# Kernel tuning notes

Measured on AMD Instinct MI355X. Metric: run time of the kernel, lower is better.

The kernel has to match this reference:

```python
import jax, jax.numpy as jnp
import numpy as np

N, E, D, IN_DIM, NUM_CLASSES, G, L = 50000, 800000, 128, 128, 10, 64, 3
BN_EPS = 1e-5


def _bn(h, gamma, beta, mean, var):
    # inference-mode batchnorm with running stats
    return (h - mean) * jax.lax.rsqrt(var + BN_EPS) * gamma + beta


def setup_inputs() -> dict:
    key = jax.random.key(0)
    ks = jax.random.split(key, 24)
    s = 0.02
    x = jax.random.normal(ks[0], (N, IN_DIM), dtype=jnp.float32)
    c_2 = jax.random.randint(ks[1], (E,), 0, N)
    u_2 = jax.random.randint(ks[2], (E,), 0, N)
    batch = jnp.sort(jax.random.randint(ks[3], (N,), 0, G))
    inp = {
        "x": x, "c_2": c_2, "u_2": u_2, "batch": batch,
        "We": jax.random.normal(ks[4], (IN_DIM, D)) * s,
        "be": jnp.zeros((D,), jnp.float32),
        # per-layer GIN MLP: Linear(d,2d) -> BN(2d) -> ReLU -> Linear(2d,d)
        "W1": jax.random.normal(ks[5], (L, D, 2 * D)) * s,
        "b1": jnp.zeros((L, 2 * D), jnp.float32),
        "g1": jnp.ones((L, 2 * D), jnp.float32),
        "bt1": jnp.zeros((L, 2 * D), jnp.float32),
        "m1": jax.random.normal(ks[6], (L, 2 * D)) * 0.1,
        "v1": jax.random.uniform(ks[7], (L, 2 * D), minval=0.5, maxval=1.5),
        "W2": jax.random.normal(ks[8], (L, 2 * D, D)) * s,
        "b2": jnp.zeros((L, D), jnp.float32),
        # post-conv BatchNorm(d)
        "g2": jnp.ones((L, D), jnp.float32),
        "bt2": jnp.zeros((L, D), jnp.float32),
        "m2": jax.random.normal(ks[9], (L, D)) * 0.1,
        "v2": jax.random.uniform(ks[10], (L, D), minval=0.5, maxval=1.5),
        # readout: Linear(d,d) -> ReLU -> (dropout off) -> Linear(d,num_classes)
        "Wr1": jax.random.normal(ks[11], (D, D)) * s,
        "br1": jnp.zeros((D,), jnp.float32),
        "Wr2": jax.random.normal(ks[12], (D, NUM_CLASSES)) * s,
        "br2": jnp.zeros((NUM_CLASSES,), jnp.float32),
    }
    return inp


def reference(x, c_2, u_2, batch, We, be, W1, b1, g1, bt1, m1, v1,
              W2, b2, g2, bt2, m2, v2, Wr1, br1, Wr2, br2):
    h = x @ We + be  # [N, D]
    for l in range(L):
        # GINConv (eps=0): h_i <- MLP(h_i + sum_{j->i} h_j)
        agg = jax.ops.segment_sum(h[c_2], u_2, num_segments=N)  # [N, D]
        z = h + agg
        z = jax.nn.relu(_bn(z @ W1[l] + b1[l], g1[l], bt1[l], m1[l], v1[l]))
        z = z @ W2[l] + b2[l]
        h = jax.nn.relu(_bn(z, g2[l], bt2[l], m2[l], v2[l]))
        # dropout: identity in eval mode
    pooled = jax.ops.segment_sum(h, batch, num_segments=G)  # [G, D]
    out = jax.nn.relu(pooled @ Wr1 + br1) @ Wr2 + br2  # [G, num_classes]
    return out
```

## Files before the change

kernel.cpp:

```cpp
#include <hip/hip_runtime.h>

#define BN_EPS 1e-5f

typedef __attribute__((ext_vector_type(8))) short bf16x8;
typedef __attribute__((ext_vector_type(4))) float f32x4;
typedef unsigned int uint32;

__device__ __forceinline__ unsigned short f2bf(float f) {
    unsigned u = __float_as_uint(f);
    u += 0x7FFFu + ((u >> 16) & 1u);
    return (unsigned short)(u >> 16);
}
__device__ __forceinline__ float bf2f(unsigned short u) {
    return __uint_as_float((unsigned)u << 16);
}
__device__ __forceinline__ float lo_bf(uint32 u) { return __uint_as_float(u << 16); }
__device__ __forceinline__ float hi_bf(uint32 u) { return __uint_as_float(u & 0xFFFF0000u); }
__device__ __forceinline__ uint32 pack_bf(float a0, float a1) {
    return ((uint32)f2bf(a1) << 16) | (uint32)f2bf(a0);
}

__global__ __launch_bounds__(256) void count_coarse_kernel(const int* __restrict__ u2,
                                                           int* __restrict__ coarse_cnt, int E) {
    __shared__ int lcnt[256];
    const int tid = threadIdx.x;
    lcnt[tid] = 0;
    __syncthreads();
    const int e0 = blockIdx.x * 4096;
#pragma unroll
    for (int k = 0; k < 16; ++k) {
        int e = e0 + k * 256 + tid;
        if (e < E) atomicAdd(&lcnt[u2[e] >> 8], 1);
    }
    __syncthreads();
    int c = lcnt[tid];
    if (c) atomicAdd(&coarse_cnt[tid], c);
}

__global__ __launch_bounds__(256) void scan_coarse_kernel(const int* __restrict__ coarse_cnt,
                                                          int* __restrict__ coarse_start,
                                                          int* __restrict__ coarse_cursor,
                                                          int nc, int total) {
    __shared__ int buf[256];
    const int t = threadIdx.x;
    int v = (t < nc) ? coarse_cnt[t] : 0;
    buf[t] = v;
    __syncthreads();
    for (int off = 1; off < 256; off <<= 1) {
        int x = (t >= off) ? buf[t - off] : 0;
        __syncthreads();
        buf[t] += x;
        __syncthreads();
    }
    int excl = buf[t] - v;
    if (t <= nc) coarse_start[t] = (t < nc) ? excl : total;
    if (t < nc) coarse_cursor[t] = excl;
}

__global__ __launch_bounds__(256) void bin_coarse_kernel(const int* __restrict__ u2,
                                                         const int* __restrict__ c2,
                                                         int* __restrict__ coarse_cursor,
                                                         int* __restrict__ buck, int E) {
    __shared__ int lcnt[256];
    __shared__ int lbase[256];
    const int tid = threadIdx.x;
    lcnt[tid] = 0;
    __syncthreads();
    const int e0 = blockIdx.x * 4096;
    int ue[16];
#pragma unroll
    for (int k = 0; k < 16; ++k) {
        int e = e0 + k * 256 + tid;
        int u = (e < E) ? u2[e] : -1;
        ue[k] = u;
        if (u >= 0) atomicAdd(&lcnt[u >> 8], 1);
    }
    __syncthreads();
    int c0 = lcnt[tid];
    lbase[tid] = c0 ? atomicAdd(&coarse_cursor[tid], c0) : 0;
    lcnt[tid] = 0;
    __syncthreads();
#pragma unroll
    for (int k = 0; k < 16; ++k) {
        int e = e0 + k * 256 + tid;
        if (e < E) {
            int u = ue[k];
            int cb = u >> 8;
            int pos = lbase[cb] + atomicAdd(&lcnt[cb], 1);
            buck[pos] = ((u & 255) << 16) | c2[e];
        }
    }
}

__global__ __launch_bounds__(256) void bin_node_kernel(const int* __restrict__ coarse_start,
                                                       const int* __restrict__ buck,
                                                       int* __restrict__ node_start,
                                                       int* __restrict__ csr_src, int N) {
    __shared__ int lcnt[256];
    __shared__ int lcur[256];
    const int cb = blockIdx.x;
    const int tid = threadIdx.x;
    const int s = coarse_start[cb];
    const int t_end = coarse_start[cb + 1];
    lcnt[tid] = 0;
    __syncthreads();
    for (int e = s + tid; e < t_end; e += 256)
        atomicAdd(&lcnt[buck[e] >> 16], 1);
    __syncthreads();
    int v = lcnt[tid];
    lcur[tid] = v;
    __syncthreads();
    for (int off = 1; off < 256; off <<= 1) {
        int x = (tid >= off) ? lcur[tid - off] : 0;
        __syncthreads();
        lcur[tid] += x;
        __syncthreads();
    }
    int excl = lcur[tid] - v;
    int gstart = s + excl;
    int idx = cb * 256 + tid;
    if (idx <= N) node_start[idx] = gstart;
    lcur[tid] = gstart;
    __syncthreads();
    for (int e = s + tid; e < t_end; e += 256) {
        int w = buck[e];
        int pos = atomicAdd(&lcur[w >> 16], 1);
        csr_src[pos] = w & 0xFFFF;
    }
}

__global__ __launch_bounds__(256) void aggregate_kernel(const unsigned short* __restrict__ h,
                                                        const int* __restrict__ row_start,
                                                        const int* __restrict__ csr_src,
                                                        unsigned short* __restrict__ h2, int N) {
    int node = blockIdx.x * 4 + (threadIdx.x >> 6);
    int lane = threadIdx.x & 63;
    if (node >= N) return;
    const int q = lane >> 4, sl = lane & 15;

    float a0 = 0.f, a1 = 0.f, a2 = 0.f, a3 = 0.f, a4 = 0.f, a5 = 0.f, a6 = 0.f, a7 = 0.f;
    if (q == 0) {
        uint4 v = ((const uint4*)(h + (size_t)node * 128))[sl];
        a0 = lo_bf(v.x); a1 = hi_bf(v.x); a2 = lo_bf(v.y); a3 = hi_bf(v.y);
        a4 = lo_bf(v.z); a5 = hi_bf(v.z); a6 = lo_bf(v.w); a7 = hi_bf(v.w);
    }

    const int rs = row_start[node], re = row_start[node + 1];
    int e = rs;
    for (; e + 16 <= re; e += 16) {
        int s0 = csr_src[e + q];
        int s1 = csr_src[e + 4 + q];
        int s2 = csr_src[e + 8 + q];
        int s3 = csr_src[e + 12 + q];
        uint4 v0 = ((const uint4*)(h + (size_t)s0 * 128))[sl];
        uint4 v1 = ((const uint4*)(h + (size_t)s1 * 128))[sl];
        uint4 v2 = ((const uint4*)(h + (size_t)s2 * 128))[sl];
        uint4 v3 = ((const uint4*)(h + (size_t)s3 * 128))[sl];
        a0 += (lo_bf(v0.x) + lo_bf(v1.x)) + (lo_bf(v2.x) + lo_bf(v3.x));
        a1 += (hi_bf(v0.x) + hi_bf(v1.x)) + (hi_bf(v2.x) + hi_bf(v3.x));
        a2 += (lo_bf(v0.y) + lo_bf(v1.y)) + (lo_bf(v2.y) + lo_bf(v3.y));
        a3 += (hi_bf(v0.y) + hi_bf(v1.y)) + (hi_bf(v2.y) + hi_bf(v3.y));
        a4 += (lo_bf(v0.z) + lo_bf(v1.z)) + (lo_bf(v2.z) + lo_bf(v3.z));
        a5 += (hi_bf(v0.z) + hi_bf(v1.z)) + (hi_bf(v2.z) + hi_bf(v3.z));
        a6 += (lo_bf(v0.w) + lo_bf(v1.w)) + (lo_bf(v2.w) + lo_bf(v3.w));
        a7 += (hi_bf(v0.w) + hi_bf(v1.w)) + (hi_bf(v2.w) + hi_bf(v3.w));
    }
    for (; e + 8 <= re; e += 8) {
        int s0 = csr_src[e + q];
        int s1 = csr_src[e + 4 + q];
        uint4 v = ((const uint4*)(h + (size_t)s0 * 128))[sl];
        uint4 w = ((const uint4*)(h + (size_t)s1 * 128))[sl];
        a0 += lo_bf(v.x) + lo_bf(w.x); a1 += hi_bf(v.x) + hi_bf(w.x);
        a2 += lo_bf(v.y) + lo_bf(w.y); a3 += hi_bf(v.y) + hi_bf(w.y);
        a4 += lo_bf(v.z) + lo_bf(w.z); a5 += hi_bf(v.z) + hi_bf(w.z);
        a6 += lo_bf(v.w) + lo_bf(w.w); a7 += hi_bf(v.w) + hi_bf(w.w);
    }
    for (; e + 4 <= re; e += 4) {
        int s0 = csr_src[e + q];
        uint4 v = ((const uint4*)(h + (size_t)s0 * 128))[sl];
        a0 += lo_bf(v.x); a1 += hi_bf(v.x); a2 += lo_bf(v.y); a3 += hi_bf(v.y);
        a4 += lo_bf(v.z); a5 += hi_bf(v.z); a6 += lo_bf(v.w); a7 += hi_bf(v.w);
    }
    if (q < re - e) {
        int s0 = csr_src[e + q];
        uint4 v = ((const uint4*)(h + (size_t)s0 * 128))[sl];
        a0 += lo_bf(v.x); a1 += hi_bf(v.x); a2 += lo_bf(v.y); a3 += hi_bf(v.y);
        a4 += lo_bf(v.z); a5 += hi_bf(v.z); a6 += lo_bf(v.w); a7 += hi_bf(v.w);
    }

    a0 += __shfl_xor(a0, 16, 64); a0 += __shfl_xor(a0, 32, 64);
    a1 += __shfl_xor(a1, 16, 64); a1 += __shfl_xor(a1, 32, 64);
    a2 += __shfl_xor(a2, 16, 64); a2 += __shfl_xor(a2, 32, 64);
    a3 += __shfl_xor(a3, 16, 64); a3 += __shfl_xor(a3, 32, 64);
    a4 += __shfl_xor(a4, 16, 64); a4 += __shfl_xor(a4, 32, 64);
    a5 += __shfl_xor(a5, 16, 64); a5 += __shfl_xor(a5, 32, 64);
    a6 += __shfl_xor(a6, 16, 64); a6 += __shfl_xor(a6, 32, 64);
    a7 += __shfl_xor(a7, 16, 64); a7 += __shfl_xor(a7, 32, 64);

    if (q == 0) {
        uint4 o;
        o.x = pack_bf(a0, a1); o.y = pack_bf(a2, a3);
        o.z = pack_bf(a4, a5); o.w = pack_bf(a6, a7);
        ((uint4*)(h2 + (size_t)node * 128))[sl] = o;
    }
}

__global__ void prep_kernel(const float* __restrict__ We, const float* __restrict__ W1,
                            const float* __restrict__ W2,
                            unsigned short* __restrict__ Wte,
                            unsigned short* __restrict__ Wt1,
                            unsigned short* __restrict__ Wt2,
                            const float* __restrict__ be,
                            const float* __restrict__ b1, const float* __restrict__ g1,
                            const float* __restrict__ bt1, const float* __restrict__ m1,
                            const float* __restrict__ v1,
                            const float* __restrict__ b2, const float* __restrict__ g2,
                            const float* __restrict__ bt2, const float* __restrict__ m2,
                            const float* __restrict__ v2,
                            float* __restrict__ sce, float* __restrict__ she,
                            float* __restrict__ sc1, float* __restrict__ sh1,
                            float* __restrict__ sc2, float* __restrict__ sh2, int L) {
    int y = blockIdx.y;
    int t = threadIdx.x;
    if (blockIdx.x == 0) {
        if (y == 0) {
            if (t < 128) { sce[t] = 1.f; she[t] = be[t]; }
        } else if (y <= L) {
            int o = (y - 1) * 256 + t;
            float s = g1[o] * rsqrtf(v1[o] + BN_EPS);
            sc1[o] = s;
            sh1[o] = (b1[o] - m1[o]) * s + bt1[o];
        } else {
            if (t < 128) {
                int o = (y - L - 1) * 128 + t;
                float s = g2[o] * rsqrtf(v2[o] + BN_EPS);
                sc2[o] = s;
                sh2[o] = (b2[o] - m2[o]) * s + bt2[o];
            }
        }
    }
    const float* src;
    unsigned short* dst;
    int K;
    if (y == 0)      { src = We; dst = Wte; K = 128; }
    else if (y <= L) { int l = y - 1;     src = W1 + (size_t)l * 128 * 256; dst = Wt1 + (size_t)l * 128 * 256; K = 128; }
    else             { int l = y - L - 1; src = W2 + (size_t)l * 256 * 128; dst = Wt2 + (size_t)l * 256 * 128; K = 256; }
    int idx = blockIdx.x * 256 + t;
    int OUT = 32768 / K;
    if (y == 0) { if (idx >= 128 * 128) return; OUT = 128; }
    int c = idx / K, k = idx % K;
    unsigned byte = ((unsigned)(idx * 2)) ^ (((unsigned)c & 7u) << 4);
    *(unsigned short*)((char*)dst + byte) = f2bf(src[(size_t)k * OUT + c]);
}

template <int K, int OUT, bool RELU, bool A_F32>
__global__ __launch_bounds__(256) void mfma_gemm_kernel(
    const void* __restrict__ Ap, const unsigned short* __restrict__ Wt,
    const float* __restrict__ scale, const float* __restrict__ shift,
    unsigned short* __restrict__ Cout, int nrows)
{
    constexpr int NT = OUT / 16;
    constexpr int KS = K / 32;
    constexpr int CH = OUT * K / 8;
    __shared__ unsigned short WtLds[OUT * K];

    const int tid = threadIdx.x;
    const int wv = tid >> 6, lane = tid & 63;
    {
#pragma unroll
        for (int i = 0; i < CH / 256; ++i) {
            unsigned chunk = (unsigned)(i * 256 + wv * 64);
            const char* gsrc = (const char*)Wt + (size_t)(chunk + lane) * 16u;
            char* ldst = (char*)WtLds + (size_t)chunk * 16u;
            __builtin_amdgcn_global_load_lds(
                (const __attribute__((address_space(1))) void*)gsrc,
                (__attribute__((address_space(3))) void*)ldst,
                16, 0, 0);
        }
    }

    const int l15 = lane & 15, lhi = lane >> 4;
    const int rbase = blockIdx.x * 128 + wv * 32;
    const int r0 = rbase + l15;
    const int r1 = rbase + 16 + l15;
    const int rr0 = min(r0, nrows - 1);
    const int rr1 = min(r1, nrows - 1);

    bf16x8 bfrag[2][KS];
    if constexpr (A_F32) {
        const float* a0 = (const float*)Ap + (size_t)rr0 * K + lhi * 8;
        const float* a1 = (const float*)Ap + (size_t)rr1 * K + lhi * 8;
#pragma unroll
        for (int ks = 0; ks < KS; ++ks) {
            float4 u0 = *(const float4*)(a0 + ks * 32);
            float4 u1 = *(const float4*)(a0 + ks * 32 + 4);
            float4 w0 = *(const float4*)(a1 + ks * 32);
            float4 w1 = *(const float4*)(a1 + ks * 32 + 4);
            bf16x8 f, g;
            f[0] = (short)f2bf(u0.x); f[1] = (short)f2bf(u0.y);
            f[2] = (short)f2bf(u0.z); f[3] = (short)f2bf(u0.w);
            f[4] = (short)f2bf(u1.x); f[5] = (short)f2bf(u1.y);
            f[6] = (short)f2bf(u1.z); f[7] = (short)f2bf(u1.w);
            g[0] = (short)f2bf(w0.x); g[1] = (short)f2bf(w0.y);
            g[2] = (short)f2bf(w0.z); g[3] = (short)f2bf(w0.w);
            g[4] = (short)f2bf(w1.x); g[5] = (short)f2bf(w1.y);
            g[6] = (short)f2bf(w1.z); g[7] = (short)f2bf(w1.w);
            bfrag[0][ks] = f;
            bfrag[1][ks] = g;
        }
    } else {
        const unsigned short* a0 = (const unsigned short*)Ap + (size_t)rr0 * K + lhi * 8;
        const unsigned short* a1 = (const unsigned short*)Ap + (size_t)rr1 * K + lhi * 8;
#pragma unroll
        for (int ks = 0; ks < KS; ++ks) {
            bfrag[0][ks] = *(const bf16x8*)(a0 + ks * 32);
            bfrag[1][ks] = *(const bf16x8*)(a1 + ks * 32);
        }
    }

    __syncthreads();

    f32x4 acc[2][NT];
#pragma unroll
    for (int g = 0; g < 2; ++g)
#pragma unroll
        for (int nt = 0; nt < NT; ++nt) acc[g][nt] = (f32x4){0.f, 0.f, 0.f, 0.f};

#pragma unroll
    for (int ks = 0; ks < KS; ++ks) {
#pragma unroll
        for (int nt = 0; nt < NT; ++nt) {
            int row = nt * 16 + l15;
            unsigned off = ((unsigned)((row * K + ks * 32 + lhi * 8) * 2)) ^ (((unsigned)(l15 & 7u)) << 4);
            bf16x8 wfrag = *(const bf16x8*)((const char*)WtLds + off);
            acc[0][nt] = __builtin_amdgcn_mfma_f32_16x16x32_bf16(wfrag, bfrag[0][ks], acc[0][nt], 0, 0, 0);
            acc[1][nt] = __builtin_amdgcn_mfma_f32_16x16x32_bf16(wfrag, bfrag[1][ks], acc[1][nt], 0, 0, 0);
        }
    }

    const float4* sc4 = (const float4*)scale;
    const float4* sh4 = (const float4*)shift;
#pragma unroll
    for (int g = 0; g < 2; ++g) {
        const int r = (g == 0) ? r0 : r1;
        if (r >= nrows) continue;
#pragma unroll
        for (int nt = 0; nt < NT; ++nt) {
            float4 sc = sc4[nt * 4 + lhi];
            float4 sh = sh4[nt * 4 + lhi];
            float y0 = acc[g][nt][0] * sc.x + sh.x;
            float y1 = acc[g][nt][1] * sc.y + sh.y;
            float y2 = acc[g][nt][2] * sc.z + sh.z;
            float y3 = acc[g][nt][3] * sc.w + sh.w;
            if (RELU) {
                y0 = fmaxf(y0, 0.f); y1 = fmaxf(y1, 0.f);
                y2 = fmaxf(y2, 0.f); y3 = fmaxf(y3, 0.f);
            }
            size_t o = (size_t)r * OUT + nt * 16 + lhi * 4;
            ushort4 p = make_ushort4(f2bf(y0), f2bf(y1), f2bf(y2), f2bf(y3));
            *(ushort4*)(Cout + o) = p;
        }
    }
}

__global__ __launch_bounds__(128) void pool_kernel(const unsigned short* __restrict__ h,
                                                   const int* __restrict__ batch,
                                                   float* __restrict__ pooled, int N, int chunk) {
    int d = threadIdx.x;
    int start = blockIdx.x * chunk;
    if (start >= N) return;
    int end = min(start + chunk, N);
    float acc = 0.f;
    int g = batch[start];
    for (int r = start; r < end; ++r) {
        int bg = batch[r];
        if (bg != g) {
            atomicAdd(&pooled[g * 128 + d], acc);
            acc = 0.f;
            g = bg;
        }
        acc += bf2f(h[(size_t)r * 128 + d]);
    }
    atomicAdd(&pooled[g * 128 + d], acc);
}

__global__ __launch_bounds__(128) void readout_kernel(const float* __restrict__ pooled,
                                                      const float* __restrict__ Wr1,
                                                      const float* __restrict__ br1,
                                                      const float* __restrict__ Wr2,
                                                      const float* __restrict__ br2,
                                                      float* __restrict__ out) {
    __shared__ float prow[128];
    __shared__ float t[128];
    int g = blockIdx.x, j = threadIdx.x;
    prow[j] = pooled[g * 128 + j];
    __syncthreads();
    float acc = 0.f;
    for (int k = 0; k < 128; ++k) acc += prow[k] * Wr1[k * 128 + j];
    t[j] = fmaxf(acc + br1[j], 0.f);
    __syncthreads();
    if (j < 10) {
        float a2 = 0.f;
        for (int k = 0; k < 128; ++k) a2 += t[k] * Wr2[k * 10 + j];
        out[g * 10 + j] = a2 + br2[j];
    }
}

extern "C" void kernel_launch(void* const* d_in, const int* in_sizes, int n_in,
                              void* d_out, int out_size, void* d_ws, size_t ws_size,
                              hipStream_t stream) {
    const float* x   = (const float*)d_in[0];
    const int* c2    = (const int*)d_in[1];
    const int* u2    = (const int*)d_in[2];
    const int* batch = (const int*)d_in[3];
    const float* We  = (const float*)d_in[4];
    const float* be  = (const float*)d_in[5];
    const float* W1  = (const float*)d_in[6];
    const float* b1  = (const float*)d_in[7];
    const float* g1  = (const float*)d_in[8];
    const float* bt1 = (const float*)d_in[9];
    const float* m1  = (const float*)d_in[10];
    const float* v1  = (const float*)d_in[11];
    const float* W2  = (const float*)d_in[12];
    const float* b2  = (const float*)d_in[13];
    const float* g2  = (const float*)d_in[14];
    const float* bt2 = (const float*)d_in[15];
    const float* m2  = (const float*)d_in[16];
    const float* v2  = (const float*)d_in[17];
    const float* Wr1 = (const float*)d_in[18];
    const float* br1 = (const float*)d_in[19];
    const float* Wr2 = (const float*)d_in[20];
    const float* br2 = (const float*)d_in[21];

    const int N = in_sizes[3];
    const int E = in_sizes[1];
    const int L = in_sizes[7] / 256;
    const int G = out_size / 10;

    const int NC = (N + 255) / 256;

    char* ws = (char*)d_ws;
    size_t off = 0;
    auto alloc = [&](size_t bytes) { char* p = ws + off; off += (bytes + 255) & ~(size_t)255; return p; };
    unsigned short* hb   = (unsigned short*)alloc((size_t)N * 128 * 2);
    unsigned short* h2b  = (unsigned short*)alloc((size_t)N * 128 * 2);
    unsigned short* zb   = (unsigned short*)alloc((size_t)N * 256 * 2);
    unsigned short* Wte  = (unsigned short*)alloc(128 * 128 * 2);
    unsigned short* Wt1  = (unsigned short*)alloc((size_t)L * 256 * 128 * 2);
    unsigned short* Wt2  = (unsigned short*)alloc((size_t)L * 128 * 256 * 2);
    float* sce = (float*)alloc(128 * 4);
    float* she = (float*)alloc(128 * 4);
    float* sc1 = (float*)alloc((size_t)L * 256 * 4);
    float* sh1 = (float*)alloc((size_t)L * 256 * 4);
    float* sc2 = (float*)alloc((size_t)L * 128 * 4);
    float* sh2 = (float*)alloc((size_t)L * 128 * 4);
    float* pooled = (float*)alloc((size_t)G * 128 * 4);
    int* coarse_cnt    = (int*)alloc(256 * 4);
    int* coarse_start  = (int*)alloc(257 * 4);
    int* coarse_cursor = (int*)alloc(256 * 4);
    int* node_start    = (int*)alloc((size_t)(N + 1) * 4);
    int* buck          = (int*)alloc((size_t)E * 4);
    int* csr_src       = (int*)alloc((size_t)E * 4);

    const int ebins = (E + 4095) / 4096;

    hipMemsetAsync(coarse_cnt, 0, 256 * 4, stream);
    hipMemsetAsync(pooled, 0, (size_t)G * 128 * 4, stream);
    count_coarse_kernel<<<ebins, 256, 0, stream>>>(u2, coarse_cnt, E);
    scan_coarse_kernel<<<1, 256, 0, stream>>>(coarse_cnt, coarse_start, coarse_cursor, NC, E);
    bin_coarse_kernel<<<ebins, 256, 0, stream>>>(u2, c2, coarse_cursor, buck, E);
    bin_node_kernel<<<NC, 256, 0, stream>>>(coarse_start, buck, node_start, csr_src, N);

    prep_kernel<<<dim3((256 * 128 + 255) / 256, 1 + 2 * L), 256, 0, stream>>>(
        We, W1, W2, Wte, Wt1, Wt2,
        be, b1, g1, bt1, m1, v1, b2, g2, bt2, m2, v2,
        sce, she, sc1, sh1, sc2, sh2, L);

    const int gemm_blocks = (N + 127) / 128;

    mfma_gemm_kernel<128, 128, false, true><<<gemm_blocks, 256, 0, stream>>>(
        x, Wte, sce, she, hb, N);

    for (int l = 0; l < L; ++l) {
        aggregate_kernel<<<(N + 3) / 4, 256, 0, stream>>>(hb, node_start, csr_src, h2b, N);
        mfma_gemm_kernel<128, 256, true, false><<<gemm_blocks, 256, 0, stream>>>(
            h2b, Wt1 + (size_t)l * 128 * 256, sc1 + l * 256, sh1 + l * 256, zb, N);
        mfma_gemm_kernel<256, 128, true, false><<<gemm_blocks, 256, 0, stream>>>(
            zb, Wt2 + (size_t)l * 256 * 128, sc2 + l * 128, sh2 + l * 128, hb, N);
    }

    const int pool_blocks = 2048;
    const int chunk = (N + pool_blocks - 1) / pool_blocks;
    pool_kernel<<<pool_blocks, 128, 0, stream>>>(hb, batch, pooled, N, chunk);
    readout_kernel<<<G, 128, 0, stream>>>(pooled, Wr1, br1, Wr2, br2, (float*)d_out);
}
```

Before: 277.6 us.

## Fuse neighbor aggregation into first MLP GEMM and drop the scan kernel

Neighbor aggregation now runs inside the first GEMM kernel. Each lane gathers and sums its row's neighbor features directly into MFMA B-fragments, so the h2b intermediate is no longer written and re-read. The separate coarse-scan kernel is removed, and each binning block redoes the small 256-entry scan itself. The cost is a gather with lower memory parallelism: one lane walks each node's edges serially, with far fewer rows per block than the wave-per-node aggregate. That may hurt latency hiding.

```diff
diff --git a/kernel.cpp b/kernel.cpp
--- a/kernel.cpp
+++ b/kernel.cpp
@@ -18,6 +18,13 @@
 __device__ __forceinline__ float hi_bf(uint32 u) { return __uint_as_float(u & 0xFFFF0000u); }
 __device__ __forceinline__ uint32 pack_bf(float a0, float a1) {
     return ((uint32)f2bf(a1) << 16) | (uint32)f2bf(a0);
+}
+
+__device__ __forceinline__ void acc8(float (&a)[8], uint4 v) {
+    a[0] += lo_bf(v.x); a[1] += hi_bf(v.x);
+    a[2] += lo_bf(v.y); a[3] += hi_bf(v.y);
+    a[4] += lo_bf(v.z); a[5] += hi_bf(v.z);
+    a[6] += lo_bf(v.w); a[7] += hi_bf(v.w);
 }
 
 __global__ __launch_bounds__(256) void count_coarse_kernel(const int* __restrict__ u2,
@@ -37,33 +44,25 @@
     if (c) atomicAdd(&coarse_cnt[tid], c);
 }
 
-__global__ __launch_bounds__(256) void scan_coarse_kernel(const int* __restrict__ coarse_cnt,
-                                                          int* __restrict__ coarse_start,
-                                                          int* __restrict__ coarse_cursor,
-                                                          int nc, int total) {
-    __shared__ int buf[256];
-    const int t = threadIdx.x;
-    int v = (t < nc) ? coarse_cnt[t] : 0;
-    buf[t] = v;
-    __syncthreads();
-    for (int off = 1; off < 256; off <<= 1) {
-        int x = (t >= off) ? buf[t - off] : 0;
-        __syncthreads();
-        buf[t] += x;
-        __syncthreads();
-    }
-    int excl = buf[t] - v;
-    if (t <= nc) coarse_start[t] = (t < nc) ? excl : total;
-    if (t < nc) coarse_cursor[t] = excl;
-}
-
 __global__ __launch_bounds__(256) void bin_coarse_kernel(const int* __restrict__ u2,
                                                          const int* __restrict__ c2,
-                                                         int* __restrict__ coarse_cursor,
-                                                         int* __restrict__ buck, int E) {
+                                                         const int* __restrict__ coarse_cnt,
+                                                         int* __restrict__ coarse_alloc,
+                                                         int* __restrict__ buck, int E, int nc) {
+    __shared__ int sbuf[256];
     __shared__ int lcnt[256];
     __shared__ int lbase[256];
     const int tid = threadIdx.x;
+    int cv = (tid < nc) ? coarse_cnt[tid] : 0;
+    sbuf[tid] = cv;
+    __syncthreads();
+    for (int off = 1; off < 256; off <<= 1) {
+        int x = (tid >= off) ? sbuf[tid - off] : 0;
+        __syncthreads();
+        sbuf[tid] += x;
+        __syncthreads();
+    }
+    const int cstart = sbuf[tid] - cv;
     lcnt[tid] = 0;
     __syncthreads();
     const int e0 = blockIdx.x * 4096;
@@ -77,7 +76,7 @@
     }
     __syncthreads();
     int c0 = lcnt[tid];
-    lbase[tid] = c0 ? atomicAdd(&coarse_cursor[tid], c0) : 0;
+    lbase[tid] = cstart + (c0 ? atomicAdd(&coarse_alloc[tid], c0) : 0);
     lcnt[tid] = 0;
     __syncthreads();
 #pragma unroll
@@ -92,18 +91,28 @@
     }
 }
 
-__global__ __launch_bounds__(256) void bin_node_kernel(const int* __restrict__ coarse_start,
+__global__ __launch_bounds__(256) void bin_node_kernel(const int* __restrict__ coarse_cnt,
                                                        const int* __restrict__ buck,
                                                        int* __restrict__ node_start,
-                                                       int* __restrict__ csr_src, int N) {
+                                                       int* __restrict__ csr_src, int N, int nc) {
+    __shared__ int sbuf[256];
     __shared__ int lcnt[256];
     __shared__ int lcur[256];
     const int cb = blockIdx.x;
     const int tid = threadIdx.x;
-    const int s = coarse_start[cb];
-    const int t_end = coarse_start[cb + 1];
+    int cv = (tid < nc) ? coarse_cnt[tid] : 0;
+    sbuf[tid] = cv;
+    __syncthreads();
+    for (int off = 1; off < 256; off <<= 1) {
+        int x = (tid >= off) ? sbuf[tid - off] : 0;
+        __syncthreads();
+        sbuf[tid] += x;
+        __syncthreads();
+    }
     lcnt[tid] = 0;
     __syncthreads();
+    const int s = (cb == 0) ? 0 : sbuf[cb - 1];
+    const int t_end = sbuf[cb];
     for (int e = s + tid; e < t_end; e += 256)
         atomicAdd(&lcnt[buck[e] >> 16], 1);
     __syncthreads();
@@ -126,82 +135,6 @@
         int w = buck[e];
         int pos = atomicAdd(&lcur[w >> 16], 1);
         csr_src[pos] = w & 0xFFFF;
-    }
-}
-
-__global__ __launch_bounds__(256) void aggregate_kernel(const unsigned short* __restrict__ h,
-                                                        const int* __restrict__ row_start,
-                                                        const int* __restrict__ csr_src,
-                                                        unsigned short* __restrict__ h2, int N) {
-    int node = blockIdx.x * 4 + (threadIdx.x >> 6);
-    int lane = threadIdx.x & 63;
-    if (node >= N) return;
-    const int q = lane >> 4, sl = lane & 15;
-
-    float a0 = 0.f, a1 = 0.f, a2 = 0.f, a3 = 0.f, a4 = 0.f, a5 = 0.f, a6 = 0.f, a7 = 0.f;
-    if (q == 0) {
-        uint4 v = ((const uint4*)(h + (size_t)node * 128))[sl];
-        a0 = lo_bf(v.x); a1 = hi_bf(v.x); a2 = lo_bf(v.y); a3 = hi_bf(v.y);
-        a4 = lo_bf(v.z); a5 = hi_bf(v.z); a6 = lo_bf(v.w); a7 = hi_bf(v.w);
-    }
-
-    const int rs = row_start[node], re = row_start[node + 1];
-    int e = rs;
-    for (; e + 16 <= re; e += 16) {
-        int s0 = csr_src[e + q];
-        int s1 = csr_src[e + 4 + q];
-        int s2 = csr_src[e + 8 + q];
-        int s3 = csr_src[e + 12 + q];
-        uint4 v0 = ((const uint4*)(h + (size_t)s0 * 128))[sl];
-        uint4 v1 = ((const uint4*)(h + (size_t)s1 * 128))[sl];
-        uint4 v2 = ((const uint4*)(h + (size_t)s2 * 128))[sl];
-        uint4 v3 = ((const uint4*)(h + (size_t)s3 * 128))[sl];
-        a0 += (lo_bf(v0.x) + lo_bf(v1.x)) + (lo_bf(v2.x) + lo_bf(v3.x));
-        a1 += (hi_bf(v0.x) + hi_bf(v1.x)) + (hi_bf(v2.x) + hi_bf(v3.x));
-        a2 += (lo_bf(v0.y) + lo_bf(v1.y)) + (lo_bf(v2.y) + lo_bf(v3.y));
-        a3 += (hi_bf(v0.y) + hi_bf(v1.y)) + (hi_bf(v2.y) + hi_bf(v3.y));
-        a4 += (lo_bf(v0.z) + lo_bf(v1.z)) + (lo_bf(v2.z) + lo_bf(v3.z));
-        a5 += (hi_bf(v0.z) + hi_bf(v1.z)) + (hi_bf(v2.z) + hi_bf(v3.z));
-        a6 += (lo_bf(v0.w) + lo_bf(v1.w)) + (lo_bf(v2.w) + lo_bf(v3.w));
-        a7 += (hi_bf(v0.w) + hi_bf(v1.w)) + (hi_bf(v2.w) + hi_bf(v3.w));
-    }
-    for (; e + 8 <= re; e += 8) {
-        int s0 = csr_src[e + q];
-        int s1 = csr_src[e + 4 + q];
-        uint4 v = ((const uint4*)(h + (size_t)s0 * 128))[sl];
-        uint4 w = ((const uint4*)(h + (size_t)s1 * 128))[sl];
-        a0 += lo_bf(v.x) + lo_bf(w.x); a1 += hi_bf(v.x) + hi_bf(w.x);
-        a2 += lo_bf(v.y) + lo_bf(w.y); a3 += hi_bf(v.y) + hi_bf(w.y);
-        a4 += lo_bf(v.z) + lo_bf(w.z); a5 += hi_bf(v.z) + hi_bf(w.z);
-        a6 += lo_bf(v.w) + lo_bf(w.w); a7 += hi_bf(v.w) + hi_bf(w.w);
-    }
-    for (; e + 4 <= re; e += 4) {
-        int s0 = csr_src[e + q];
-        uint4 v = ((const uint4*)(h + (size_t)s0 * 128))[sl];
-        a0 += lo_bf(v.x); a1 += hi_bf(v.x); a2 += lo_bf(v.y); a3 += hi_bf(v.y);
-        a4 += lo_bf(v.z); a5 += hi_bf(v.z); a6 += lo_bf(v.w); a7 += hi_bf(v.w);
-    }
-    if (q < re - e) {
-        int s0 = csr_src[e + q];
-        uint4 v = ((const uint4*)(h + (size_t)s0 * 128))[sl];
-        a0 += lo_bf(v.x); a1 += hi_bf(v.x); a2 += lo_bf(v.y); a3 += hi_bf(v.y);
-        a4 += lo_bf(v.z); a5 += hi_bf(v.z); a6 += lo_bf(v.w); a7 += hi_bf(v.w);
-    }
-
-    a0 += __shfl_xor(a0, 16, 64); a0 += __shfl_xor(a0, 32, 64);
-    a1 += __shfl_xor(a1, 16, 64); a1 += __shfl_xor(a1, 32, 64);
-    a2 += __shfl_xor(a2, 16, 64); a2 += __shfl_xor(a2, 32, 64);
-    a3 += __shfl_xor(a3, 16, 64); a3 += __shfl_xor(a3, 32, 64);
-    a4 += __shfl_xor(a4, 16, 64); a4 += __shfl_xor(a4, 32, 64);
-    a5 += __shfl_xor(a5, 16, 64); a5 += __shfl_xor(a5, 32, 64);
-    a6 += __shfl_xor(a6, 16, 64); a6 += __shfl_xor(a6, 32, 64);
-    a7 += __shfl_xor(a7, 16, 64); a7 += __shfl_xor(a7, 32, 64);
-
-    if (q == 0) {
-        uint4 o;
-        o.x = pack_bf(a0, a1); o.y = pack_bf(a2, a3);
-        o.z = pack_bf(a4, a5); o.w = pack_bf(a6, a7);
-        ((uint4*)(h2 + (size_t)node * 128))[sl] = o;
     }
 }
 
@@ -253,6 +186,139 @@
     *(unsigned short*)((char*)dst + byte) = f2bf(src[(size_t)k * OUT + c]);
 }
 
+__global__ __launch_bounds__(256) void agg_gemm_kernel(
+    const unsigned short* __restrict__ h,
+    const int* __restrict__ node_start,
+    const int* __restrict__ csr_src,
+    const unsigned short* __restrict__ Wt,
+    const float* __restrict__ scale, const float* __restrict__ shift,
+    unsigned short* __restrict__ Cout, int nrows)
+{
+    constexpr int K = 128, OUT = 256;
+    constexpr int NT = OUT / 16;
+    constexpr int KS = K / 32;
+    constexpr int CH = OUT * K / 8;
+    __shared__ unsigned short WtLds[OUT * K];
+
+    const int tid = threadIdx.x;
+    const int wv = tid >> 6, lane = tid & 63;
+    {
+#pragma unroll
+        for (int i = 0; i < CH / 256; ++i) {
+            unsigned chunk = (unsigned)(i * 256 + wv * 64);
+            const char* gsrc = (const char*)Wt + (size_t)(chunk + lane) * 16u;
+            char* ldst = (char*)WtLds + (size_t)chunk * 16u;
+            __builtin_amdgcn_global_load_lds(
+                (const __attribute__((address_space(1))) void*)gsrc,
+                (__attribute__((address_space(3))) void*)ldst,
+                16, 0, 0);
+        }
+    }
+
+    const int l15 = lane & 15, lhi = lane >> 4;
+    const int rbase = blockIdx.x * 128 + wv * 32;
+    const char* hb8 = (const char*)h;
+    const unsigned off0 = (unsigned)lhi * 16u;
+
+    bf16x8 bfrag[2][KS];
+#pragma unroll
+    for (int g = 0; g < 2; ++g) {
+        const int r = rbase + g * 16 + l15;
+        const int rr = min(r, nrows - 1);
+        const char* selfp = hb8 + (size_t)rr * 256 + off0;
+        float a0[8], a1[8], a2[8], a3[8];
+        {
+            uint4 v0 = *(const uint4*)(selfp);
+            uint4 v1 = *(const uint4*)(selfp + 64);
+            uint4 v2 = *(const uint4*)(selfp + 128);
+            uint4 v3 = *(const uint4*)(selfp + 192);
+            a0[0] = lo_bf(v0.x); a0[1] = hi_bf(v0.x); a0[2] = lo_bf(v0.y); a0[3] = hi_bf(v0.y);
+            a0[4] = lo_bf(v0.z); a0[5] = hi_bf(v0.z); a0[6] = lo_bf(v0.w); a0[7] = hi_bf(v0.w);
+            a1[0] = lo_bf(v1.x); a1[1] = hi_bf(v1.x); a1[2] = lo_bf(v1.y); a1[3] = hi_bf(v1.y);
+            a1[4] = lo_bf(v1.z); a1[5] = hi_bf(v1.z); a1[6] = lo_bf(v1.w); a1[7] = hi_bf(v1.w);
+            a2[0] = lo_bf(v2.x); a2[1] = hi_bf(v2.x); a2[2] = lo_bf(v2.y); a2[3] = hi_bf(v2.y);
+            a2[4] = lo_bf(v2.z); a2[5] = hi_bf(v2.z); a2[6] = lo_bf(v2.w); a2[7] = hi_bf(v2.w);
+            a3[0] = lo_bf(v3.x); a3[1] = hi_bf(v3.x); a3[2] = lo_bf(v3.y); a3[3] = hi_bf(v3.y);
+            a3[4] = lo_bf(v3.z); a3[5] = hi_bf(v3.z); a3[6] = lo_bf(v3.w); a3[7] = hi_bf(v3.w);
+        }
+        int e = node_start[rr];
+        const int re = node_start[rr + 1];
+        for (; e + 2 <= re; e += 2) {
+            int s0 = csr_src[e], s1 = csr_src[e + 1];
+            const char* p0 = hb8 + (size_t)s0 * 256 + off0;
+            const char* p1 = hb8 + (size_t)s1 * 256 + off0;
+            uint4 u0 = *(const uint4*)(p0);
+            uint4 u1 = *(const uint4*)(p0 + 64);
+            uint4 u2 = *(const uint4*)(p0 + 128);
+            uint4 u3 = *(const uint4*)(p0 + 192);
+            uint4 w0 = *(const uint4*)(p1);
+            uint4 w1 = *(const uint4*)(p1 + 64);
+            uint4 w2 = *(const uint4*)(p1 + 128);
+            uint4 w3 = *(const uint4*)(p1 + 192);
+            acc8(a0, u0); acc8(a1, u1); acc8(a2, u2); acc8(a3, u3);
+            acc8(a0, w0); acc8(a1, w1); acc8(a2, w2); acc8(a3, w3);
+        }
+        if (e < re) {
+            int s0 = csr_src[e];
+            const char* p0 = hb8 + (size_t)s0 * 256 + off0;
+            uint4 u0 = *(const uint4*)(p0);
+            uint4 u1 = *(const uint4*)(p0 + 64);
+            uint4 u2 = *(const uint4*)(p0 + 128);
+            uint4 u3 = *(const uint4*)(p0 + 192);
+            acc8(a0, u0); acc8(a1, u1); acc8(a2, u2); acc8(a3, u3);
+        }
+        bf16x8 f0, f1, f2, f3;
+#pragma unroll
+        for (int j = 0; j < 8; ++j) {
+            f0[j] = (short)f2bf(a0[j]);
+            f1[j] = (short)f2bf(a1[j]);
+            f2[j] = (short)f2bf(a2[j]);
+            f3[j] = (short)f2bf(a3[j]);
+        }
+        bfrag[g][0] = f0; bfrag[g][1] = f1; bfrag[g][2] = f2; bfrag[g][3] = f3;
+    }
+
+    __syncthreads();
+
+    f32x4 acc[2][NT];
+#pragma unroll
+    for (int g = 0; g < 2; ++g)
+#pragma unroll
+        for (int nt = 0; nt < NT; ++nt) acc[g][nt] = (f32x4){0.f, 0.f, 0.f, 0.f};
+
+#pragma unroll
+    for (int ks = 0; ks < KS; ++ks) {
+#pragma unroll
+        for (int nt = 0; nt < NT; ++nt) {
+            int row = nt * 16 + l15;
+            unsigned off = ((unsigned)((row * K + ks * 32 + lhi * 8) * 2)) ^ (((unsigned)(l15 & 7u)) << 4);
+            bf16x8 wfrag = *(const bf16x8*)((const char*)WtLds + off);
+            acc[0][nt] = __builtin_amdgcn_mfma_f32_16x16x32_bf16(wfrag, bfrag[0][ks], acc[0][nt], 0, 0, 0);
+            acc[1][nt] = __builtin_amdgcn_mfma_f32_16x16x32_bf16(wfrag, bfrag[1][ks], acc[1][nt], 0, 0, 0);
+        }
+    }
+
+    const float4* sc4 = (const float4*)scale;
+    const float4* sh4 = (const float4*)shift;
+#pragma unroll
+    for (int g = 0; g < 2; ++g) {
+        const int r = rbase + g * 16 + l15;
+        if (r >= nrows) continue;
+#pragma unroll
+        for (int nt = 0; nt < NT; ++nt) {
+            float4 sc = sc4[nt * 4 + lhi];
+            float4 sh = sh4[nt * 4 + lhi];
+            float y0 = fmaxf(acc[g][nt][0] * sc.x + sh.x, 0.f);
+            float y1 = fmaxf(acc[g][nt][1] * sc.y + sh.y, 0.f);
+            float y2 = fmaxf(acc[g][nt][2] * sc.z + sh.z, 0.f);
+            float y3 = fmaxf(acc[g][nt][3] * sc.w + sh.w, 0.f);
+            size_t o = (size_t)r * OUT + nt * 16 + lhi * 4;
+            ushort4 p = make_ushort4(f2bf(y0), f2bf(y1), f2bf(y2), f2bf(y3));
+            *(ushort4*)(Cout + o) = p;
+        }
+    }
+}
+
 template <int K, int OUT, bool RELU, bool A_F32>
 __global__ __launch_bounds__(256) void mfma_gemm_kernel(
     const void* __restrict__ Ap, const unsigned short* __restrict__ Wt,
@@ -443,7 +509,6 @@
     size_t off = 0;
     auto alloc = [&](size_t bytes) { char* p = ws + off; off += (bytes + 255) & ~(size_t)255; return p; };
     unsigned short* hb   = (unsigned short*)alloc((size_t)N * 128 * 2);
-    unsigned short* h2b  = (unsigned short*)alloc((size_t)N * 128 * 2);
     unsigned short* zb   = (unsigned short*)alloc((size_t)N * 256 * 2);
     unsigned short* Wte  = (unsigned short*)alloc(128 * 128 * 2);
     unsigned short* Wt1  = (unsigned short*)alloc((size_t)L * 256 * 128 * 2);
@@ -455,21 +520,19 @@
     float* sc2 = (float*)alloc((size_t)L * 128 * 4);
     float* sh2 = (float*)alloc((size_t)L * 128 * 4);
     float* pooled = (float*)alloc((size_t)G * 128 * 4);
-    int* coarse_cnt    = (int*)alloc(256 * 4);
-    int* coarse_start  = (int*)alloc(257 * 4);
-    int* coarse_cursor = (int*)alloc(256 * 4);
-    int* node_start    = (int*)alloc((size_t)(N + 1) * 4);
-    int* buck          = (int*)alloc((size_t)E * 4);
-    int* csr_src       = (int*)alloc((size_t)E * 4);
+    int* coarse_cnt   = (int*)alloc(512 * 4);
+    int* coarse_alloc = coarse_cnt + 256;
+    int* node_start   = (int*)alloc((size_t)(N + 1) * 4);
+    int* buck         = (int*)alloc((size_t)E * 4);
+    int* csr_src      = (int*)alloc((size_t)E * 4);
 
     const int ebins = (E + 4095) / 4096;
 
-    hipMemsetAsync(coarse_cnt, 0, 256 * 4, stream);
+    hipMemsetAsync(coarse_cnt, 0, 512 * 4, stream);
     hipMemsetAsync(pooled, 0, (size_t)G * 128 * 4, stream);
     count_coarse_kernel<<<ebins, 256, 0, stream>>>(u2, coarse_cnt, E);
-    scan_coarse_kernel<<<1, 256, 0, stream>>>(coarse_cnt, coarse_start, coarse_cursor, NC, E);
-    bin_coarse_kernel<<<ebins, 256, 0, stream>>>(u2, c2, coarse_cursor, buck, E);
-    bin_node_kernel<<<NC, 256, 0, stream>>>(coarse_start, buck, node_start, csr_src, N);
+    bin_coarse_kernel<<<ebins, 256, 0, stream>>>(u2, c2, coarse_cnt, coarse_alloc, buck, E, NC);
+    bin_node_kernel<<<NC, 256, 0, stream>>>(coarse_cnt, buck, node_start, csr_src, N, NC);
 
     prep_kernel<<<dim3((256 * 128 + 255) / 256, 1 + 2 * L), 256, 0, stream>>>(
         We, W1, W2, Wte, Wt1, Wt2,
@@ -482,9 +545,9 @@
         x, Wte, sce, she, hb, N);
 
     for (int l = 0; l < L; ++l) {
-        aggregate_kernel<<<(N + 3) / 4, 256, 0, stream>>>(hb, node_start, csr_src, h2b, N);
-        mfma_gemm_kernel<128, 256, true, false><<<gemm_blocks, 256, 0, stream>>>(
-            h2b, Wt1 + (size_t)l * 128 * 256, sc1 + l * 256, sh1 + l * 256, zb, N);
+        agg_gemm_kernel<<<gemm_blocks, 256, 0, stream>>>(
+            hb, node_start, csr_src,
+            Wt1 + (size_t)l * 128 * 256, sc1 + l * 256, sh1 + l * 256, zb, N);
         mfma_gemm_kernel<256, 128, true, false><<<gemm_blocks, 256, 0, stream>>>(
             zb, Wt2 + (size_t)l * 256 * 128, sc2 + l * 128, sh2 + l * 128, hb, N);
     }
```

Measured after the change: 376.7 us, median of 2. 35.7% more time.
